# Kernel optimization log

Hardware: AMD Instinct MI355X
Metric: run time of the kernel (lower is better)

The kernel has to match this reference:

```python
import jax, jax.numpy as jnp
import numpy as np

GROUP_SIZE = 64
BITS = 4
VALS_PER_WORD = 32 // BITS  # 8 nibbles per uint32


def setup_inputs() -> dict:
    key = jax.random.key(0)
    ks = jax.random.split(key, 7)
    B, S, I, O = 4, 2048, 4096, 4096
    G = I // GROUP_SIZE
    x = jax.random.normal(ks[0], (B, S, I), dtype=jnp.float32)
    channel_scale = jax.random.uniform(ks[1], (1, 1, I), dtype=jnp.float32, minval=0.5, maxval=1.5)
    # packed int4 weights: random uint32 words
    qweight = jax.random.randint(ks[2], (O, I // VALS_PER_WORD), 0, 2147483647, dtype=jnp.int32).astype(jnp.uint32)
    q_perm = jax.random.permutation(ks[3], I).astype(jnp.int32)
    scales = jax.random.uniform(ks[4], (O, G), dtype=jnp.float32, minval=0.001, maxval=0.02)
    zeros = jax.random.normal(ks[5], (O, G), dtype=jnp.float32) * 0.05
    bias = jax.random.normal(ks[6], (O,), dtype=jnp.float32) * 0.02
    return {"x": x, "channel_scale": channel_scale, "qweight": qweight,
            "q_perm": q_perm, "scales": scales, "zeros": zeros, "bias": bias}


def _dequantize(qweight, scales, zeros):
    # qweight: (O, I/8) uint32 -> nibbles little-endian within each word
    O, packed = qweight.shape
    shifts = (jnp.arange(VALS_PER_WORD, dtype=jnp.uint32) * BITS)  # (8,)
    wq = (qweight[:, :, None] >> shifts[None, None, :]) & jnp.uint32((1 << BITS) - 1)
    wq = wq.reshape(O, packed * VALS_PER_WORD).astype(jnp.float32)  # (O, I)
    # mlx dequantize: w = wq * scale + bias(zeros), per group of GROUP_SIZE along input dim
    s = jnp.repeat(scales, GROUP_SIZE, axis=1)  # (O, I)
    z = jnp.repeat(zeros, GROUP_SIZE, axis=1)   # (O, I)
    return wq * s + z


def reference(x, channel_scale, qweight, q_perm, scales, zeros, bias):
    # per-channel scale
    x = x * channel_scale
    # optional permute gather along feature axis
    x = jnp.take(x, q_perm, axis=-1)
    # group-wise int4 dequant matmul (transpose=True: out = x @ W^T)
    W = _dequantize(qweight, scales, zeros)  # (O, I)
    out = jnp.einsum('bsi,oi->bso', x, W)
    return out + bias
```

## Files before the change

### kernel.cpp

```cpp
#include <hip/hip_runtime.h>
#include <hip/hip_bf16.h>

typedef unsigned short u16;
typedef unsigned int u32;
typedef unsigned char u8;

#define M_DIM 8192
#define K_DIM 4096
#define N_DIM 4096
#define GROUPS 64

typedef int intx4 __attribute__((ext_vector_type(4)));

__device__ __forceinline__ void gload_lds16(const void* g, void* l) {
  __builtin_amdgcn_global_load_lds(
      (const __attribute__((address_space(1))) void*)g,
      (__attribute__((address_space(3))) void*)l, 16, 0, 0);
}

__device__ __forceinline__ float block_absmax(float amax, float* red) {
#pragma unroll
  for (int off = 32; off; off >>= 1)
    amax = fmaxf(amax, __shfl_xor(amax, off, 64));
  const int wave = threadIdx.x >> 6;
  if ((threadIdx.x & 63) == 0) red[wave] = amax;
  __syncthreads();
  return fmaxf(fmaxf(red[0], red[1]), fmaxf(red[2], red[3]));
}

__device__ __forceinline__ u32 pack4(const float* v, float inv) {
  u32 r = 0;
#pragma unroll
  for (int i = 0; i < 4; ++i) {
    int q = (int)__builtin_rintf(v[i] * inv);
    q = q > 127 ? 127 : (q < -127 ? -127 : q);
    r |= ((u32)(u8)(char)q) << (8 * i);
  }
  return r;
}

__global__ __launch_bounds__(256) void prep_x(
    const float* __restrict__ x, const float* __restrict__ cs,
    const int* __restrict__ perm, u8* __restrict__ xq, float* __restrict__ sx) {
  __shared__ float row[K_DIM];
  __shared__ float red[4];
  const size_t m = blockIdx.x;
  const float* xr = x + m * K_DIM;
  const int t = threadIdx.x;
  float amax = 0.f;
#pragma unroll
  for (int j = 0; j < 16; ++j) {
    const int idx = j * 256 + t;
    float v = xr[idx] * cs[idx];
    amax = fmaxf(amax, fabsf(v));
    row[idx] = v;
  }
  amax = block_absmax(amax, red);
  amax = fmaxf(amax, 1e-20f);
  const float inv = 127.0f / amax;
  const int base = t * 16;
  int4 p0 = *(const int4*)(perm + base + 0);
  int4 p1 = *(const int4*)(perm + base + 4);
  int4 p2 = *(const int4*)(perm + base + 8);
  int4 p3 = *(const int4*)(perm + base + 12);
  float g[16];
  g[0]  = row[p0.x]; g[1]  = row[p0.y]; g[2]  = row[p0.z]; g[3]  = row[p0.w];
  g[4]  = row[p1.x]; g[5]  = row[p1.y]; g[6]  = row[p1.z]; g[7]  = row[p1.w];
  g[8]  = row[p2.x]; g[9]  = row[p2.y]; g[10] = row[p2.z]; g[11] = row[p2.w];
  g[12] = row[p3.x]; g[13] = row[p3.y]; g[14] = row[p3.z]; g[15] = row[p3.w];
  uint4 pk;
  pk.x = pack4(g + 0, inv);
  pk.y = pack4(g + 4, inv);
  pk.z = pack4(g + 8, inv);
  pk.w = pack4(g + 12, inv);
  *(uint4*)(xq + m * K_DIM + base) = pk;
  if (t == 0) sx[m] = amax * (1.0f / 127.0f);
}

__global__ __launch_bounds__(256) void prep_w(
    const u32* __restrict__ qw,
    const float* __restrict__ scales, const float* __restrict__ zeros,
    u8* __restrict__ wq, float* __restrict__ sw) {
  __shared__ float red[4];
  const int o = blockIdx.x;
  const u32* qrow = qw + (size_t)o * (K_DIM / 8);
  const int t = threadIdx.x;
  const float s = scales[o * GROUPS + (t >> 2)];
  const float z = zeros[o * GROUPS + (t >> 2)];
  uint2 w = *(const uint2*)(qrow + 2 * t);
  float v[16];
  float amax = 0.f;
#pragma unroll
  for (int n = 0; n < 8; ++n) {
    v[n]     = (float)((w.x >> (4 * n)) & 15u) * s + z;
    v[8 + n] = (float)((w.y >> (4 * n)) & 15u) * s + z;
    amax = fmaxf(amax, fmaxf(fabsf(v[n]), fabsf(v[8 + n])));
  }
  amax = block_absmax(amax, red);
  amax = fmaxf(amax, 1e-20f);
  const float inv = 127.0f / amax;
  uint4 p;
  p.x = pack4(v + 0, inv);
  p.y = pack4(v + 4, inv);
  p.z = pack4(v + 8, inv);
  p.w = pack4(v + 12, inv);
  *(uint4*)(wq + (size_t)o * K_DIM + t * 16) = p;
  if (t == 0) sw[o] = amax * (1.0f / 127.0f);
}

#define BM 256
#define BN 256
#define BK 64
#define KTILES (K_DIM / BK)

__global__ __launch_bounds__(512, 2) void gemm_i8(
    const u8* __restrict__ A, const u8* __restrict__ B,
    const float* __restrict__ sx, const float* __restrict__ sw,
    const float* __restrict__ bias, float* __restrict__ out) {
  __shared__ __align__(16) u8 As[3][BM * BK];
  __shared__ __align__(16) u8 Bs[3][BN * BK];
  const int tid = threadIdx.x;
  const int lane = tid & 63;
  const int wave = tid >> 6;
  const int wm = wave >> 2;
  const int wn = wave & 3;
  const int q = lane >> 4, lr = lane & 15;
  const int qs = q ^ ((lr >> 1) & 3);
  const int blockN = blockIdx.x * BN;
  const int blockM = blockIdx.y * BM;

  const char* Abase = (const char*)(A + (size_t)blockM * K_DIM);
  const char* Bbase = (const char*)(B + (size_t)blockN * K_DIM);

  const int c0 = tid, c1 = tid + 512;
  const int kc0 = (c0 & 3) ^ ((c0 >> 3) & 3);
  const int kc1 = (c1 & 3) ^ ((c1 >> 3) & 3);
  const size_t gOff0 = (size_t)(c0 >> 2) * K_DIM + kc0 * 16;
  const size_t gOff1 = (size_t)(c1 >> 2) * K_DIM + kc1 * 16;
  const int dOff0 = c0 * 16, dOff1 = c1 * 16;

  const int aoff = (wm * 128 + lr) * 64 + qs * 16;
  const int boff = (wn * 64 + lr) * 64 + qs * 16;

  intx4 acc[8][4];
#pragma unroll
  for (int i = 0; i < 8; ++i)
#pragma unroll
    for (int j = 0; j < 4; ++j) acc[i][j] = (intx4)0;

  gload_lds16(Abase + gOff0, &As[0][dOff0]);
  gload_lds16(Abase + gOff1, &As[0][dOff1]);
  gload_lds16(Bbase + gOff0, &Bs[0][dOff0]);
  gload_lds16(Bbase + gOff1, &Bs[0][dOff1]);
  gload_lds16(Abase + gOff0 + BK, &As[1][dOff0]);
  gload_lds16(Abase + gOff1 + BK, &As[1][dOff1]);
  gload_lds16(Bbase + gOff0 + BK, &Bs[1][dOff0]);
  gload_lds16(Bbase + gOff1 + BK, &Bs[1][dOff1]);
  asm volatile("s_waitcnt vmcnt(4)" ::: "memory");
  asm volatile("s_barrier" ::: "memory");

  int bc = 0, bs = 2;
  for (int t = 0; t < KTILES; ++t) {
    const u8* Ab = &As[bc][0];
    const u8* Bb = &Bs[bc][0];
    u8* Aw = &As[bs][0];
    u8* Bw = &Bs[bs][0];
    const size_t koff2 = (size_t)(t + 2) * BK;
    const bool pf = (t + 2 < KTILES);
    intx4 bf[4], a0, a1;

#define MFMA8(MI0, MI1)                                                     \
  __builtin_amdgcn_s_setprio(1);                                            \
  _Pragma("unroll") for (int ni = 0; ni < 4; ++ni)                          \
      acc[MI0][ni] = __builtin_amdgcn_mfma_i32_16x16x64_i8(                 \
          a0, bf[ni], acc[MI0][ni], 0, 0, 0);                               \
  _Pragma("unroll") for (int ni = 0; ni < 4; ++ni)                          \
      acc[MI1][ni] = __builtin_amdgcn_mfma_i32_16x16x64_i8(                 \
          a1, bf[ni], acc[MI1][ni], 0, 0, 0);                               \
  __builtin_amdgcn_s_setprio(0);

    bf[0] = *(const intx4*)(Bb + boff + 0 * 1024);
    bf[1] = *(const intx4*)(Bb + boff + 1 * 1024);
    bf[2] = *(const intx4*)(Bb + boff + 2 * 1024);
    bf[3] = *(const intx4*)(Bb + boff + 3 * 1024);
    a0 = *(const intx4*)(Ab + aoff + 0 * 1024);
    a1 = *(const intx4*)(Ab + aoff + 1 * 1024);
    if (pf) gload_lds16(Abase + gOff0 + koff2, Aw + dOff0);
    asm volatile("s_barrier" ::: "memory");
    MFMA8(0, 1)
    asm volatile("s_barrier" ::: "memory");

    a0 = *(const intx4*)(Ab + aoff + 2 * 1024);
    a1 = *(const intx4*)(Ab + aoff + 3 * 1024);
    if (pf) gload_lds16(Abase + gOff1 + koff2, Aw + dOff1);
    asm volatile("s_barrier" ::: "memory");
    MFMA8(2, 3)
    asm volatile("s_barrier" ::: "memory");

    a0 = *(const intx4*)(Ab + aoff + 4 * 1024);
    a1 = *(const intx4*)(Ab + aoff + 5 * 1024);
    if (pf) gload_lds16(Bbase + gOff0 + koff2, Bw + dOff0);
    asm volatile("s_barrier" ::: "memory");
    MFMA8(4, 5)
    asm volatile("s_barrier" ::: "memory");

    a0 = *(const intx4*)(Ab + aoff + 6 * 1024);
    a1 = *(const intx4*)(Ab + aoff + 7 * 1024);
    if (pf) gload_lds16(Bbase + gOff1 + koff2, Bw + dOff1);
    asm volatile("s_barrier" ::: "memory");
    MFMA8(6, 7)
    if (t < KTILES - 2) {
      asm volatile("s_waitcnt vmcnt(4)" ::: "memory");
    } else if (t == KTILES - 2) {
      asm volatile("s_waitcnt vmcnt(0)" ::: "memory");
    }
    if (t < KTILES - 1) asm volatile("s_barrier" ::: "memory");

    bc = (bc == 2) ? 0 : bc + 1;
    bs = (bs == 2) ? 0 : bs + 1;
#undef MFMA8
  }

#pragma unroll
  for (int ni = 0; ni < 4; ++ni) {
    const int col = blockN + wn * 64 + ni * 16 + lr;
    const float swv = sw[col];
    const float bv = bias[col];
#pragma unroll
    for (int mi = 0; mi < 8; ++mi) {
      const int row0 = blockM + wm * 128 + mi * 16 + q * 4;
#pragma unroll
      for (int r = 0; r < 4; ++r) {
        const float s = sx[row0 + r] * swv;
        out[(size_t)(row0 + r) * N_DIM + col] = (float)acc[mi][ni][r] * s + bv;
      }
    }
  }
}

extern "C" void kernel_launch(void* const* d_in, const int* in_sizes, int n_in,
                              void* d_out, int out_size, void* d_ws, size_t ws_size,
                              hipStream_t stream) {
  const float* x      = (const float*)d_in[0];
  const float* cs     = (const float*)d_in[1];
  const u32*   qw     = (const u32*)d_in[2];
  const int*   perm   = (const int*)d_in[3];
  const float* scales = (const float*)d_in[4];
  const float* zeros  = (const float*)d_in[5];
  const float* bias   = (const float*)d_in[6];
  float* out = (float*)d_out;

  u8* xq = (u8*)d_ws;
  u8* wq = xq + (size_t)M_DIM * K_DIM;
  float* sx = (float*)(wq + (size_t)N_DIM * K_DIM);
  float* sw = sx + M_DIM;

  hipLaunchKernelGGL(prep_x, dim3(M_DIM), dim3(256), 0, stream, x, cs, perm, xq, sx);
  hipLaunchKernelGGL(prep_w, dim3(N_DIM), dim3(256), 0, stream,
                     qw, scales, zeros, wq, sw);
  hipLaunchKernelGGL(gemm_i8, dim3(N_DIM / BN, M_DIM / BM), dim3(512), 0,
                     stream, xq, wq, sx, sw, bias, out);
}
```

Baseline: 414.4 us.

## Move permutation onto weights, fuse prep kernels, switch GEMM to 32x32 MFMA

The gather permutation is moved off the activations and onto the weight rows: each weight row is scattered by q_perm into LDS, so x is quantized with contiguous vectorized float4 loads and no LDS gather. Both prep kernels are merged into one launch. The int8 GEMM now uses 32x32x32 MFMA with 16-wide accumulators, which cuts LDS fragment loads and barriers per K-tile. Correctness depends on the inverse-permutation equivalence and the new LDS swizzle and output layout matching.

```diff
diff --git a/kernel.cpp b/kernel.cpp
--- a/kernel.cpp
+++ b/kernel.cpp
@@ -1,7 +1,5 @@
 #include <hip/hip_runtime.h>
-#include <hip/hip_bf16.h>
-
-typedef unsigned short u16;
+
 typedef unsigned int u32;
 typedef unsigned char u8;
 
@@ -11,6 +9,7 @@
 #define GROUPS 64
 
 typedef int intx4 __attribute__((ext_vector_type(4)));
+typedef int intx16 __attribute__((ext_vector_type(16)));
 
 __device__ __forceinline__ void gload_lds16(const void* g, void* l) {
   __builtin_amdgcn_global_load_lds(
@@ -39,73 +38,79 @@
   return r;
 }
 
-__global__ __launch_bounds__(256) void prep_x(
+__global__ __launch_bounds__(256) void prep_all(
     const float* __restrict__ x, const float* __restrict__ cs,
-    const int* __restrict__ perm, u8* __restrict__ xq, float* __restrict__ sx) {
-  __shared__ float row[K_DIM];
+    const u32* __restrict__ qw, const int* __restrict__ perm,
+    const float* __restrict__ scales, const float* __restrict__ zeros,
+    u8* __restrict__ xq, u8* __restrict__ wq,
+    float* __restrict__ sx, float* __restrict__ sw) {
+  __shared__ float rowbuf[K_DIM];
   __shared__ float red[4];
-  const size_t m = blockIdx.x;
-  const float* xr = x + m * K_DIM;
   const int t = threadIdx.x;
-  float amax = 0.f;
-#pragma unroll
-  for (int j = 0; j < 16; ++j) {
-    const int idx = j * 256 + t;
-    float v = xr[idx] * cs[idx];
-    amax = fmaxf(amax, fabsf(v));
-    row[idx] = v;
-  }
-  amax = block_absmax(amax, red);
-  amax = fmaxf(amax, 1e-20f);
-  const float inv = 127.0f / amax;
   const int base = t * 16;
-  int4 p0 = *(const int4*)(perm + base + 0);
-  int4 p1 = *(const int4*)(perm + base + 4);
-  int4 p2 = *(const int4*)(perm + base + 8);
-  int4 p3 = *(const int4*)(perm + base + 12);
-  float g[16];
-  g[0]  = row[p0.x]; g[1]  = row[p0.y]; g[2]  = row[p0.z]; g[3]  = row[p0.w];
-  g[4]  = row[p1.x]; g[5]  = row[p1.y]; g[6]  = row[p1.z]; g[7]  = row[p1.w];
-  g[8]  = row[p2.x]; g[9]  = row[p2.y]; g[10] = row[p2.z]; g[11] = row[p2.w];
-  g[12] = row[p3.x]; g[13] = row[p3.y]; g[14] = row[p3.z]; g[15] = row[p3.w];
-  uint4 pk;
-  pk.x = pack4(g + 0, inv);
-  pk.y = pack4(g + 4, inv);
-  pk.z = pack4(g + 8, inv);
-  pk.w = pack4(g + 12, inv);
-  *(uint4*)(xq + m * K_DIM + base) = pk;
-  if (t == 0) sx[m] = amax * (1.0f / 127.0f);
-}
-
-__global__ __launch_bounds__(256) void prep_w(
-    const u32* __restrict__ qw,
-    const float* __restrict__ scales, const float* __restrict__ zeros,
-    u8* __restrict__ wq, float* __restrict__ sw) {
-  __shared__ float red[4];
-  const int o = blockIdx.x;
-  const u32* qrow = qw + (size_t)o * (K_DIM / 8);
-  const int t = threadIdx.x;
-  const float s = scales[o * GROUPS + (t >> 2)];
-  const float z = zeros[o * GROUPS + (t >> 2)];
-  uint2 w = *(const uint2*)(qrow + 2 * t);
-  float v[16];
-  float amax = 0.f;
-#pragma unroll
-  for (int n = 0; n < 8; ++n) {
-    v[n]     = (float)((w.x >> (4 * n)) & 15u) * s + z;
-    v[8 + n] = (float)((w.y >> (4 * n)) & 15u) * s + z;
-    amax = fmaxf(amax, fmaxf(fabsf(v[n]), fabsf(v[8 + n])));
-  }
-  amax = block_absmax(amax, red);
-  amax = fmaxf(amax, 1e-20f);
-  const float inv = 127.0f / amax;
-  uint4 p;
-  p.x = pack4(v + 0, inv);
-  p.y = pack4(v + 4, inv);
-  p.z = pack4(v + 8, inv);
-  p.w = pack4(v + 12, inv);
-  *(uint4*)(wq + (size_t)o * K_DIM + t * 16) = p;
-  if (t == 0) sw[o] = amax * (1.0f / 127.0f);
+  if (blockIdx.x < N_DIM) {
+    const int o = blockIdx.x;
+    const u32* qrow = qw + (size_t)o * (K_DIM / 8);
+    const float s = scales[o * GROUPS + (t >> 2)];
+    const float z = zeros[o * GROUPS + (t >> 2)];
+    uint2 w = *(const uint2*)(qrow + 2 * t);
+    int4 p0 = *(const int4*)(perm + base + 0);
+    int4 p1 = *(const int4*)(perm + base + 4);
+    int4 p2 = *(const int4*)(perm + base + 8);
+    int4 p3 = *(const int4*)(perm + base + 12);
+    float v[16];
+    float amax = 0.f;
+#pragma unroll
+    for (int n = 0; n < 8; ++n) {
+      v[n]     = (float)((w.x >> (4 * n)) & 15u) * s + z;
+      v[8 + n] = (float)((w.y >> (4 * n)) & 15u) * s + z;
+      amax = fmaxf(amax, fmaxf(fabsf(v[n]), fabsf(v[8 + n])));
+    }
+    rowbuf[p0.x] = v[0];  rowbuf[p0.y] = v[1];
+    rowbuf[p0.z] = v[2];  rowbuf[p0.w] = v[3];
+    rowbuf[p1.x] = v[4];  rowbuf[p1.y] = v[5];
+    rowbuf[p1.z] = v[6];  rowbuf[p1.w] = v[7];
+    rowbuf[p2.x] = v[8];  rowbuf[p2.y] = v[9];
+    rowbuf[p2.z] = v[10]; rowbuf[p2.w] = v[11];
+    rowbuf[p3.x] = v[12]; rowbuf[p3.y] = v[13];
+    rowbuf[p3.z] = v[14]; rowbuf[p3.w] = v[15];
+    amax = block_absmax(amax, red);
+    amax = fmaxf(amax, 1e-20f);
+    const float inv = 127.0f / amax;
+    uint4 p;
+    p.x = pack4(rowbuf + base + 0, inv);
+    p.y = pack4(rowbuf + base + 4, inv);
+    p.z = pack4(rowbuf + base + 8, inv);
+    p.w = pack4(rowbuf + base + 12, inv);
+    *(uint4*)(wq + (size_t)o * K_DIM + base) = p;
+    if (t == 0) sw[o] = amax * (1.0f / 127.0f);
+  } else {
+    const size_t m = blockIdx.x - N_DIM;
+    const float* xr = x + m * K_DIM;
+    float v[16];
+    float amax = 0.f;
+#pragma unroll
+    for (int j = 0; j < 4; ++j) {
+      float4 xv = *(const float4*)(xr + base + j * 4);
+      float4 cv = *(const float4*)(cs + base + j * 4);
+      v[j * 4 + 0] = xv.x * cv.x;
+      v[j * 4 + 1] = xv.y * cv.y;
+      v[j * 4 + 2] = xv.z * cv.z;
+      v[j * 4 + 3] = xv.w * cv.w;
+#pragma unroll
+      for (int i = 0; i < 4; ++i) amax = fmaxf(amax, fabsf(v[j * 4 + i]));
+    }
+    amax = block_absmax(amax, red);
+    amax = fmaxf(amax, 1e-20f);
+    const float inv = 127.0f / amax;
+    uint4 p;
+    p.x = pack4(v + 0, inv);
+    p.y = pack4(v + 4, inv);
+    p.z = pack4(v + 8, inv);
+    p.w = pack4(v + 12, inv);
+    *(uint4*)(xq + m * K_DIM + base) = p;
+    if (t == 0) sx[m] = amax * (1.0f / 127.0f);
+  }
 }
 
 #define BM 256
@@ -124,8 +129,9 @@
   const int wave = tid >> 6;
   const int wm = wave >> 2;
   const int wn = wave & 3;
-  const int q = lane >> 4, lr = lane & 15;
-  const int qs = q ^ ((lr >> 1) & 3);
+  const int l5 = lane & 31;
+  const int hi = lane >> 5;
+  const int swz = (l5 >> 1) & 3;
   const int blockN = blockIdx.x * BN;
   const int blockM = blockIdx.y * BM;
 
@@ -139,14 +145,14 @@
   const size_t gOff1 = (size_t)(c1 >> 2) * K_DIM + kc1 * 16;
   const int dOff0 = c0 * 16, dOff1 = c1 * 16;
 
-  const int aoff = (wm * 128 + lr) * 64 + qs * 16;
-  const int boff = (wn * 64 + lr) * 64 + qs * 16;
-
-  intx4 acc[8][4];
-#pragma unroll
-  for (int i = 0; i < 8; ++i)
-#pragma unroll
-    for (int j = 0; j < 4; ++j) acc[i][j] = (intx4)0;
+  const int aoff = (wm * 128 + l5) * 64 + ((hi ^ swz) << 4);
+  const int boff = (wn * 64 + l5) * 64 + ((hi ^ swz) << 4);
+
+  intx16 acc[4][2];
+#pragma unroll
+  for (int i = 0; i < 4; ++i)
+#pragma unroll
+    for (int j = 0; j < 2; ++j) acc[i][j] = (intx16)0;
 
   gload_lds16(Abase + gOff0, &As[0][dOff0]);
   gload_lds16(Abase + gOff1, &As[0][dOff1]);
@@ -167,48 +173,51 @@
     u8* Bw = &Bs[bs][0];
     const size_t koff2 = (size_t)(t + 2) * BK;
     const bool pf = (t + 2 < KTILES);
-    intx4 bf[4], a0, a1;
-
-#define MFMA8(MI0, MI1)                                                     \
-  __builtin_amdgcn_s_setprio(1);                                            \
-  _Pragma("unroll") for (int ni = 0; ni < 4; ++ni)                          \
-      acc[MI0][ni] = __builtin_amdgcn_mfma_i32_16x16x64_i8(                 \
-          a0, bf[ni], acc[MI0][ni], 0, 0, 0);                               \
-  _Pragma("unroll") for (int ni = 0; ni < 4; ++ni)                          \
-      acc[MI1][ni] = __builtin_amdgcn_mfma_i32_16x16x64_i8(                 \
-          a1, bf[ni], acc[MI1][ni], 0, 0, 0);                               \
-  __builtin_amdgcn_s_setprio(0);
-
-    bf[0] = *(const intx4*)(Bb + boff + 0 * 1024);
-    bf[1] = *(const intx4*)(Bb + boff + 1 * 1024);
-    bf[2] = *(const intx4*)(Bb + boff + 2 * 1024);
-    bf[3] = *(const intx4*)(Bb + boff + 3 * 1024);
-    a0 = *(const intx4*)(Ab + aoff + 0 * 1024);
-    a1 = *(const intx4*)(Ab + aoff + 1 * 1024);
-    if (pf) gload_lds16(Abase + gOff0 + koff2, Aw + dOff0);
+
+    intx4 b00 = *(const intx4*)(Bb + boff);
+    intx4 b01 = *(const intx4*)(Bb + (boff ^ 32));
+    intx4 b10 = *(const intx4*)(Bb + boff + 2048);
+    intx4 b11 = *(const intx4*)(Bb + (boff ^ 32) + 2048);
+    intx4 a00 = *(const intx4*)(Ab + aoff);
+    intx4 a01 = *(const intx4*)(Ab + (aoff ^ 32));
+    intx4 a10 = *(const intx4*)(Ab + aoff + 2048);
+    intx4 a11 = *(const intx4*)(Ab + (aoff ^ 32) + 2048);
+    if (pf) {
+      gload_lds16(Abase + gOff0 + koff2, Aw + dOff0);
+      gload_lds16(Bbase + gOff0 + koff2, Bw + dOff0);
+    }
     asm volatile("s_barrier" ::: "memory");
-    MFMA8(0, 1)
+    __builtin_amdgcn_s_setprio(1);
+    acc[0][0] = __builtin_amdgcn_mfma_i32_32x32x32_i8(a00, b00, acc[0][0], 0, 0, 0);
+    acc[0][1] = __builtin_amdgcn_mfma_i32_32x32x32_i8(a00, b10, acc[0][1], 0, 0, 0);
+    acc[1][0] = __builtin_amdgcn_mfma_i32_32x32x32_i8(a10, b00, acc[1][0], 0, 0, 0);
+    acc[1][1] = __builtin_amdgcn_mfma_i32_32x32x32_i8(a10, b10, acc[1][1], 0, 0, 0);
+    acc[0][0] = __builtin_amdgcn_mfma_i32_32x32x32_i8(a01, b01, acc[0][0], 0, 0, 0);
+    acc[0][1] = __builtin_amdgcn_mfma_i32_32x32x32_i8(a01, b11, acc[0][1], 0, 0, 0);
+    acc[1][0] = __builtin_amdgcn_mfma_i32_32x32x32_i8(a11, b01, acc[1][0], 0, 0, 0);
+    acc[1][1] = __builtin_amdgcn_mfma_i32_32x32x32_i8(a11, b11, acc[1][1], 0, 0, 0);
+    __builtin_amdgcn_s_setprio(0);
     asm volatile("s_barrier" ::: "memory");
 
-    a0 = *(const intx4*)(Ab + aoff + 2 * 1024);
-    a1 = *(const intx4*)(Ab + aoff + 3 * 1024);
-    if (pf) gload_lds16(Abase + gOff1 + koff2, Aw + dOff1);
+    intx4 a20 = *(const intx4*)(Ab + aoff + 4096);
+    intx4 a21 = *(const intx4*)(Ab + (aoff ^ 32) + 4096);
+    intx4 a30 = *(const intx4*)(Ab + aoff + 6144);
+    intx4 a31 = *(const intx4*)(Ab + (aoff ^ 32) + 6144);
+    if (pf) {
+      gload_lds16(Abase + gOff1 + koff2, Aw + dOff1);
+      gload_lds16(Bbase + gOff1 + koff2, Bw + dOff1);
+    }
     asm volatile("s_barrier" ::: "memory");
-    MFMA8(2, 3)
-    asm volatile("s_barrier" ::: "memory");
-
-    a0 = *(const intx4*)(Ab + aoff + 4 * 1024);
-    a1 = *(const intx4*)(Ab + aoff + 5 * 1024);
-    if (pf) gload_lds16(Bbase + gOff0 + koff2, Bw + dOff0);
-    asm volatile("s_barrier" ::: "memory");
-    MFMA8(4, 5)
-    asm volatile("s_barrier" ::: "memory");
-
-    a0 = *(const intx4*)(Ab + aoff + 6 * 1024);
-    a1 = *(const intx4*)(Ab + aoff + 7 * 1024);
-    if (pf) gload_lds16(Bbase + gOff1 + koff2, Bw + dOff1);
-    asm volatile("s_barrier" ::: "memory");
-    MFMA8(6, 7)
+    __builtin_amdgcn_s_setprio(1);
+    acc[2][0] = __builtin_amdgcn_mfma_i32_32x32x32_i8(a20, b00, acc[2][0], 0, 0, 0);
+    acc[2][1] = __builtin_amdgcn_mfma_i32_32x32x32_i8(a20, b10, acc[2][1], 0, 0, 0);
+    acc[3][0] = __builtin_amdgcn_mfma_i32_32x32x32_i8(a30, b00, acc[3][0], 0, 0, 0);
+    acc[3][1] = __builtin_amdgcn_mfma_i32_32x32x32_i8(a30, b10, acc[3][1], 0, 0, 0);
+    acc[2][0] = __builtin_amdgcn_mfma_i32_32x32x32_i8(a21, b01, acc[2][0], 0, 0, 0);
+    acc[2][1] = __builtin_amdgcn_mfma_i32_32x32x32_i8(a21, b11, acc[2][1], 0, 0, 0);
+    acc[3][0] = __builtin_amdgcn_mfma_i32_32x32x32_i8(a31, b01, acc[3][0], 0, 0, 0);
+    acc[3][1] = __builtin_amdgcn_mfma_i32_32x32x32_i8(a31, b11, acc[3][1], 0, 0, 0);
+    __builtin_amdgcn_s_setprio(0);
     if (t < KTILES - 2) {
       asm volatile("s_waitcnt vmcnt(4)" ::: "memory");
     } else if (t == KTILES - 2) {
@@ -218,21 +227,24 @@
 
     bc = (bc == 2) ? 0 : bc + 1;
     bs = (bs == 2) ? 0 : bs + 1;
-#undef MFMA8
-  }
-
-#pragma unroll
-  for (int ni = 0; ni < 4; ++ni) {
-    const int col = blockN + wn * 64 + ni * 16 + lr;
+  }
+
+#pragma unroll
+  for (int ni = 0; ni < 2; ++ni) {
+    const int col = blockN + wn * 64 + ni * 32 + l5;
     const float swv = sw[col];
     const float bv = bias[col];
 #pragma unroll
-    for (int mi = 0; mi < 8; ++mi) {
-      const int row0 = blockM + wm * 128 + mi * 16 + q * 4;
-#pragma unroll
-      for (int r = 0; r < 4; ++r) {
-        const float s = sx[row0 + r] * swv;
-        out[(size_t)(row0 + r) * N_DIM + col] = (float)acc[mi][ni][r] * s + bv;
+    for (int mi = 0; mi < 4; ++mi) {
+      const int row0 = blockM + wm * 128 + mi * 32 + 4 * hi;
+#pragma unroll
+      for (int rg = 0; rg < 4; ++rg) {
+#pragma unroll
+        for (int rr = 0; rr < 4; ++rr) {
+          const int row = row0 + rg * 8 + rr;
+          const float s = sx[row] * swv;
+          out[(size_t)row * N_DIM + col] = (float)acc[mi][ni][rg * 4 + rr] * s + bv;
+        }
       }
     }
   }
@@ -255,9 +267,8 @@
   float* sx = (float*)(wq + (size_t)N_DIM * K_DIM);
   float* sw = sx + M_DIM;
 
-  hipLaunchKernelGGL(prep_x, dim3(M_DIM), dim3(256), 0, stream, x, cs, perm, xq, sx);
-  hipLaunchKernelGGL(prep_w, dim3(N_DIM), dim3(256), 0, stream,
-                     qw, scales, zeros, wq, sw);
+  hipLaunchKernelGGL(prep_all, dim3(N_DIM + M_DIM), dim3(256), 0, stream,
+                     x, cs, qw, perm, scales, zeros, xq, wq, sx, sw);
   hipLaunchKernelGGL(gemm_i8, dim3(N_DIM / BN, M_DIM / BM), dim3(512), 0,
                      stream, xq, wq, sx, sw, bias, out);
 }
```

Measured after the change: 388.5 us. 1.07x faster.
